# Kernel optimization log

Hardware: AMD Instinct MI355X
Metric: run time of the kernel (lower is better)

The kernel has to match this reference:

```python
import jax, jax.numpy as jnp
import numpy as np

N = 50000      # num_nodes
E = 800000     # num_edges (avg degree 16)
D = 128        # input_dim = hidden_dim = output_dim
L = 3          # num_layers
EPS = 1e-5     # BatchNorm eps


def setup_inputs() -> dict:
    key = jax.random.key(0)
    k_x, k_e, k_w, k_b = jax.random.split(key, 4)
    x = jax.random.normal(k_x, (N, D), dtype=jnp.float32)
    edge_index = jax.random.randint(k_e, (2, E), 0, N, dtype=jnp.int32)
    # Stacked per-layer params: GCN weight/bias + BatchNorm gamma/beta
    Ws = jax.random.normal(k_w, (L, D, D), dtype=jnp.float32) * (1.0 / np.sqrt(D))
    bs = jax.random.normal(k_b, (L, D), dtype=jnp.float32) * 0.01
    gammas = jnp.ones((L, D), dtype=jnp.float32)
    betas = jnp.zeros((L, D), dtype=jnp.float32)
    return {"x": x, "edge_index": edge_index, "Ws": Ws, "bs": bs,
            "gammas": gammas, "betas": betas}


def reference(x, edge_index, Ws, bs, gammas, betas):
    """CausalGNN forward: L x (GCNConv -> BN(train stats) -> ReLU[not last]) with residuals.
    Dropout p=0 (deterministic). GCNConv is PyG-style: add self-loops, symmetric
    D^{-1/2} (A+I) D^{-1/2} normalization, linear transform + bias."""
    src, dst = edge_index[0], edge_index[1]
    # degree including self-loop (+1), computed at aggregation index
    deg = jax.ops.segment_sum(jnp.ones((E,), jnp.float32), dst, num_segments=N) + 1.0
    dis = jax.lax.rsqrt(deg)                       # deg >= 1, safe
    norm = dis[src] * dis[dst]                      # [E] edge norm
    self_norm = dis * dis                           # [N] self-loop norm = 1/deg

    for i in range(L):
        h = x @ Ws[i]                               # [N, D]
        # scatter-add aggregation of normalized neighbor messages
        agg = jax.ops.segment_sum(h[src] * norm[:, None], dst, num_segments=N)
        agg = agg + self_norm[:, None] * h + bs[i]
        # BatchNorm1d (training mode: biased batch statistics over nodes)
        mean = jnp.mean(agg, axis=0)
        var = jnp.mean(jnp.square(agg - mean), axis=0)
        y = gammas[i] * (agg - mean) * jax.lax.rsqrt(var + EPS) + betas[i]
        if i < L - 1:
            y = jax.nn.relu(y)
        x = x + y if i > 0 else y                   # residual (dims match)
    return x
```

## Files before the change

### kernel.cpp

```cpp
#include <hip/hip_runtime.h>
#include <hip/hip_bf16.h>
#include <hip/hip_fp16.h>

#define N_ 50000
#define E_ 800000
#define D_ 128
#define L_ 3

#define GG 782
#define CB 3125

typedef _Float16 half8 __attribute__((ext_vector_type(8)));
typedef float f32x4 __attribute__((ext_vector_type(4)));


__device__ inline float4 hcvt(uint2 u) {
    __half2 h0 = *(__half2*)&u.x;
    __half2 h1 = *(__half2*)&u.y;
    float2 f0 = __half22float2(h0);
    float2 f1 = __half22float2(h1);
    return make_float4(f0.x, f0.y, f1.x, f1.y);
}

__device__ inline unsigned pkh(float a, float b) {
    __half2 h = __floats2half2_rn(a, b);
    return *(unsigned*)&h;
}

__device__ inline unsigned short pkh1(float a) {
    _Float16 h = (_Float16)a;
    return *(unsigned short*)&h;
}


__global__ void k_countw(const int* __restrict__ dst, int* __restrict__ deg,
                         int* __restrict__ offbuf,
                         const float* __restrict__ Ws, unsigned short* __restrict__ Wb) {
    int b = blockIdx.x;
    if (b < CB) {
        int e = b * 256 + threadIdx.x;
        offbuf[e] = atomicAdd(&deg[dst[e]], 1);
    } else {
        int l = b - CB;
        const float* Wl = Ws + l * 16384;
        unsigned short* Wo = Wb + l * 16384;
        for (int i = threadIdx.x; i < 16384; i += 256) {
            int n = i >> 7, k = i & 127;
            Wo[n * 128 + k] = pkh1(Wl[k * 128 + n]);
        }
    }
}


__global__ __launch_bounds__(1024) void k_scan1(const int* __restrict__ deg,
                                                int* __restrict__ linc,
                                                int* __restrict__ bsum,
                                                float* __restrict__ dis) {
    __shared__ int wsum[16];
    int t    = threadIdx.x;
    int lane = t & 63;
    int wid  = t >> 6;
    int i    = blockIdx.x * 1024 + t;
    int d    = (i < N_) ? deg[i] : 0;
    if (i < N_) dis[i] = rsqrtf((float)d + 1.0f);
    int v = d;
#pragma unroll
    for (int off = 1; off < 64; off <<= 1) {
        int u = __shfl_up(v, off);
        if (lane >= off) v += u;
    }
    if (lane == 63) wsum[wid] = v;
    __syncthreads();
    if (wid == 0) {
        int w = (lane < 16) ? wsum[lane] : 0;
#pragma unroll
        for (int off = 1; off < 16; off <<= 1) {
            int u = __shfl_up(w, off);
            if (lane >= off) w += u;
        }
        if (lane < 16) wsum[lane] = w;
    }
    __syncthreads();
    int woff = (wid > 0) ? wsum[wid - 1] : 0;
    v += woff;
    if (i < N_) linc[i] = v;
    if (t == 1023) bsum[blockIdx.x] = v;
}

__global__ __launch_bounds__(1024) void k_scan3(const int* __restrict__ linc,
                                                const int* __restrict__ bsum,
                                                int* __restrict__ row_ptr) {
    __shared__ int sboff;
    int t = threadIdx.x;
    if (t < 64) {
        int v = (t < 49) ? bsum[t] : 0;
#pragma unroll
        for (int off = 1; off < 64; off <<= 1) {
            int u = __shfl_up(v, off);
            if (t >= off) v += u;
        }
        int ex = (blockIdx.x == 0) ? 0 : __shfl(v, (int)blockIdx.x - 1, 64);
        if (t == 0) sboff = ex;
    }
    __syncthreads();
    int i = blockIdx.x * 1024 + t;
    if (i < N_) row_ptr[i + 1] = linc[i] + sboff;
    if (i == 0) row_ptr[0] = 0;
}


__device__ __forceinline__ void gemm_body(const float* __restrict__ Xin,
                                          const unsigned short* __restrict__ Wb,
                                          const float* __restrict__ dis,
                                          uint4* __restrict__ Hb,
                                          const float* __restrict__ st,
                                          const float* __restrict__ gamma,
                                          const float* __restrict__ beta,
                                          const unsigned short* __restrict__ resH,
                                          unsigned short* __restrict__ xoutH,
                                          int blk) {
    __shared__ unsigned short wt[128 * 136];
    __shared__ unsigned short xb[64 * 136];
    __shared__ float sab[256];
    int t  = threadIdx.x;
    int r0 = blk * 64;

    if (st) {
        if (t < 128) {
            float s = 0.f, s2 = 0.f;
#pragma unroll
            for (int k = 0; k < 8; ++k) {
                s  += st[k * 256 + t];
                s2 += st[k * 256 + 128 + t];
            }
            float mean = s * (1.0f / N_);
            float var  = s2 * (1.0f / N_) - mean * mean;
            float a = gamma[t] * rsqrtf(var + 1e-5f);
            sab[t]       = a;
            sab[128 + t] = beta[t] - mean * a;
        }
        __syncthreads();
    }

#pragma unroll
    for (int j = 0; j < 8; ++j) {
        int i = t + 256 * j;
        int row = i >> 4, c16 = i & 15;
        *(uint4*)&wt[row * 136 + c16 * 8] = ((const uint4*)Wb)[i];
    }
#pragma unroll
    for (int j = 0; j < 8; ++j) {
        int g   = t + 256 * j;
        int row = g >> 5;
        int c4  = (g & 31) * 4;
        int gr  = r0 + row;
        float4 v = make_float4(0.f, 0.f, 0.f, 0.f);
        if (gr < N_) {
            v = *(const float4*)(Xin + gr * 128 + c4);
            if (st) {
                v.x = fmaxf(sab[c4] * v.x + sab[128 + c4], 0.f);
                v.y = fmaxf(sab[c4 + 1] * v.y + sab[128 + c4 + 1], 0.f);
                v.z = fmaxf(sab[c4 + 2] * v.z + sab[128 + c4 + 2], 0.f);
                v.w = fmaxf(sab[c4 + 3] * v.w + sab[128 + c4 + 3], 0.f);
                if (resH) {
                    float4 rr = hcvt(*(const uint2*)(resH + gr * 128 + c4));
                    v.x += rr.x; v.y += rr.y; v.z += rr.z; v.w += rr.w;
                }
            }
        }
        uint2 p;
        p.x = pkh(v.x, v.y);
        p.y = pkh(v.z, v.w);
        if (st && gr < N_) *(uint2*)(xoutH + gr * 128 + c4) = p;
        *(uint2*)&xb[row * 136 + c4] = p;
    }
    __syncthreads();

    int wv   = t >> 6;
    int lane = t & 63;
    int ln   = lane & 15;
    int quad = lane >> 4;

    const unsigned short* arow = &xb[(wv * 16 + ln) * 136 + quad * 8];
    half8 af[4];
#pragma unroll
    for (int ks = 0; ks < 4; ++ks) af[ks] = *(const half8*)(arow + ks * 32);

    f32x4 acc[8];
#pragma unroll
    for (int ct = 0; ct < 8; ++ct) acc[ct] = (f32x4){0.f, 0.f, 0.f, 0.f};

#pragma unroll
    for (int ct = 0; ct < 8; ++ct) {
        const unsigned short* wp = &wt[(ct * 16 + ln) * 136 + quad * 8];
#pragma unroll
        for (int ks = 0; ks < 4; ++ks) {
            half8 bf = *(const half8*)(wp + ks * 32);
            acc[ct] = __builtin_amdgcn_mfma_f32_16x16x32_f16(af[ks], bf, acc[ct], 0, 0, 0);
        }
    }

    float dr[4];
#pragma unroll
    for (int reg = 0; reg < 4; ++reg) {
        int r = r0 + wv * 16 + quad * 4 + reg;
        dr[reg] = dis[r < N_ ? r : (N_ - 1)];
    }
    __syncthreads();
#pragma unroll
    for (int ct = 0; ct < 8; ++ct) {
#pragma unroll
        for (int reg = 0; reg < 4; ++reg) {
            int lrow = wv * 16 + quad * 4 + reg;
            xb[lrow * 136 + ct * 16 + ln] = pkh1(acc[ct][reg] * dr[reg]);
        }
    }
    __syncthreads();
#pragma unroll
    for (int j = 0; j < 4; ++j) {
        int i = t + 256 * j;
        int row = i >> 4, c16 = i & 15;
        int gr = r0 + row;
        if (gr < N_) Hb[gr * 16 + c16] = *(uint4*)&xb[row * 136 + c16 * 8];
    }
}


__global__ __launch_bounds__(256) void k_fillg(const int* __restrict__ src,
                                               const int* __restrict__ dst,
                                               const int* __restrict__ row_ptr,
                                               const int* __restrict__ offbuf,
                                               int* __restrict__ csr_src,
                                               const float* __restrict__ x,
                                               const unsigned short* __restrict__ Wb,
                                               const float* __restrict__ dis,
                                               uint4* __restrict__ Hb) {
    int b = blockIdx.x;
    if (b < GG) {
        gemm_body(x, Wb, dis, Hb, nullptr, nullptr, nullptr, nullptr, nullptr, b);
    } else {
        int e = (b - GG) * 256 + threadIdx.x;
        int d = dst[e];
        csr_src[row_ptr[d] + offbuf[e]] = src[e];
    }
}


__global__ __launch_bounds__(256) void k_gemm(const float* __restrict__ Xin,
                                              const unsigned short* __restrict__ Wb,
                                              const float* __restrict__ dis,
                                              uint4* __restrict__ Hb,
                                              const float* __restrict__ st,
                                              const float* __restrict__ gamma,
                                              const float* __restrict__ beta,
                                              const unsigned short* __restrict__ resH,
                                              unsigned short* __restrict__ xoutH) {
    gemm_body(Xin, Wb, dis, Hb, st, gamma, beta, resH, xoutH, blockIdx.x);
}


__global__ __launch_bounds__(256) void k_agg(const uint4* __restrict__ Hb,
                                             const int* __restrict__ row_ptr,
                                             const int* __restrict__ csr_src,
                                             const float* __restrict__ dis,
                                             const float* __restrict__ bias,
                                             float4* __restrict__ AGG,
                                             float* __restrict__ stats2) {
    int tid  = threadIdx.x;
    int sub  = tid >> 4;
    int lane = tid & 15;
    int node = blockIdx.x * 16 + sub;

    int beg = row_ptr[node], end = row_ptr[node + 1];
    uint4 su = Hb[node * 16 + lane];
    float4 acc0 = hcvt(make_uint2(su.x, su.y));
    float4 acc1 = hcvt(make_uint2(su.z, su.w));

    for (int c = beg; c < end; c += 16) {
        int m = end - c; if (m > 16) m = 16;
        int idx = (lane < m) ? csr_src[c + lane] : 0;
        int j = 0;
        for (; j + 4 <= m; j += 4) {
            int s0 = __shfl(idx, j, 16);
            int s1 = __shfl(idx, j + 1, 16);
            int s2 = __shfl(idx, j + 2, 16);
            int s3 = __shfl(idx, j + 3, 16);
            uint4 a0 = Hb[s0 * 16 + lane];
            uint4 a1 = Hb[s1 * 16 + lane];
            uint4 a2 = Hb[s2 * 16 + lane];
            uint4 a3 = Hb[s3 * 16 + lane];
            float4 f00 = hcvt(make_uint2(a0.x, a0.y)), f01 = hcvt(make_uint2(a0.z, a0.w));
            float4 f10 = hcvt(make_uint2(a1.x, a1.y)), f11 = hcvt(make_uint2(a1.z, a1.w));
            float4 f20 = hcvt(make_uint2(a2.x, a2.y)), f21 = hcvt(make_uint2(a2.z, a2.w));
            float4 f30 = hcvt(make_uint2(a3.x, a3.y)), f31 = hcvt(make_uint2(a3.z, a3.w));
            acc0.x += f00.x + f10.x + f20.x + f30.x;
            acc0.y += f00.y + f10.y + f20.y + f30.y;
            acc0.z += f00.z + f10.z + f20.z + f30.z;
            acc0.w += f00.w + f10.w + f20.w + f30.w;
            acc1.x += f01.x + f11.x + f21.x + f31.x;
            acc1.y += f01.y + f11.y + f21.y + f31.y;
            acc1.z += f01.z + f11.z + f21.z + f31.z;
            acc1.w += f01.w + f11.w + f21.w + f31.w;
        }
        for (; j < m; ++j) {
            int s0 = __shfl(idx, j, 16);
            uint4 a0 = Hb[s0 * 16 + lane];
            float4 f00 = hcvt(make_uint2(a0.x, a0.y)), f01 = hcvt(make_uint2(a0.z, a0.w));
            acc0.x += f00.x; acc0.y += f00.y; acc0.z += f00.z; acc0.w += f00.w;
            acc1.x += f01.x; acc1.y += f01.y; acc1.z += f01.z; acc1.w += f01.w;
        }
    }

    float dn = dis[node];
    float4 b0 = *(const float4*)(bias + lane * 8);
    float4 b1 = *(const float4*)(bias + lane * 8 + 4);
    float4 r0, r1;
    r0.x = dn * acc0.x + b0.x; r0.y = dn * acc0.y + b0.y;
    r0.z = dn * acc0.z + b0.z; r0.w = dn * acc0.w + b0.w;
    r1.x = dn * acc1.x + b1.x; r1.y = dn * acc1.y + b1.y;
    r1.z = dn * acc1.z + b1.z; r1.w = dn * acc1.w + b1.w;
    AGG[node * 32 + lane * 2]     = r0;
    AGG[node * 32 + lane * 2 + 1] = r1;

    __shared__ float sbuf[16][128];
    float4* sp = (float4*)&sbuf[sub][lane * 8];
    sp[0] = r0; sp[1] = r1;
    __syncthreads();
    if (tid < 128) {
        float s = 0.f, s2 = 0.f;
#pragma unroll
        for (int k = 0; k < 16; ++k) {
            float v = sbuf[k][tid];
            s += v; s2 += v * v;
        }
        float* stp = stats2 + (blockIdx.x & 7) * 256;
        atomicAdd(&stp[tid], s);
        atomicAdd(&stp[128 + tid], s2);
    }
}


__global__ __launch_bounds__(256) void k_normF(const float4* __restrict__ AGG,
                                               const unsigned short* __restrict__ resH,
                                               const float* __restrict__ st,
                                               const float* __restrict__ gamma,
                                               const float* __restrict__ beta,
                                               float4* __restrict__ OUT) {
    __shared__ float sab[256];
    int t = threadIdx.x;
    if (t < 128) {
        float s = 0.f, s2 = 0.f;
#pragma unroll
        for (int k = 0; k < 8; ++k) {
            s  += st[k * 256 + t];
            s2 += st[k * 256 + 128 + t];
        }
        float mean = s * (1.0f / N_);
        float var  = s2 * (1.0f / N_) - mean * mean;
        float a = gamma[t] * rsqrtf(var + 1e-5f);
        sab[t]       = a;
        sab[128 + t] = beta[t] - mean * a;
    }
    __syncthreads();
    for (int i = blockIdx.x * 256 + t; i < N_ * 32; i += gridDim.x * 256) {
        int f4 = (i & 31) * 4;
        float4 v = AGG[i];
        float4 rr = hcvt(((const uint2*)resH)[i]);
        v.x = sab[f4] * v.x + sab[128 + f4] + rr.x;
        v.y = sab[f4 + 1] * v.y + sab[128 + f4 + 1] + rr.y;
        v.z = sab[f4 + 2] * v.z + sab[128 + f4 + 2] + rr.z;
        v.w = sab[f4 + 3] * v.w + sab[128 + f4 + 3] + rr.w;
        OUT[i] = v;
    }
}


extern "C" void kernel_launch(void* const* d_in, const int* in_sizes, int n_in,
                              void* d_out, int out_size, void* d_ws, size_t ws_size,
                              hipStream_t stream) {
    const float* x      = (const float*)d_in[0];
    const int*   ei     = (const int*)d_in[1];
    const float* Ws     = (const float*)d_in[2];
    const float* bs     = (const float*)d_in[3];
    const float* gammas = (const float*)d_in[4];
    const float* betas  = (const float*)d_in[5];
    float* out = (float*)d_out;

    const int* src = ei;
    const int* dst = ei + E_;

    char* w = (char*)d_ws;
    int*   deg     = (int*)(w + 0);
    float* stats2  = (float*)(w + 200000);
    int*   row_ptr = (int*)(w + 224576);
    float* dis     = (float*)(w + 424592);
    int*   offbuf  = (int*)(w + 624592);
    int*   csr_src = (int*)(w + 3824592);
    uint4* Hb      = (uint4*)(w + 7024640);
    unsigned short* XBh = (unsigned short*)(w + 19824640);
    unsigned short* Wb  = (unsigned short*)(w + 32624640);
    float* AGG     = out;

    int* linc = (int*)XBh;
    int* bsum = (int*)XBh + N_;

    hipMemsetAsync(d_ws, 0, 224576, stream);

    k_countw<<<CB + 3, 256, 0, stream>>>(dst, deg, offbuf, Ws, Wb);
    k_scan1<<<49, 1024, 0, stream>>>(deg, linc, bsum, dis);
    k_scan3<<<49, 1024, 0, stream>>>(linc, bsum, row_ptr);
    k_fillg<<<GG + CB, 256, 0, stream>>>(src, dst, row_ptr, offbuf, csr_src,
                                         x, Wb, dis, Hb);

    k_agg<<<N_ / 16, 256, 0, stream>>>(Hb, row_ptr, csr_src, dis, bs,
                                       (float4*)AGG, stats2);
    k_gemm<<<GG, 256, 0, stream>>>(AGG, Wb + 16384, dis, Hb,
                                   stats2, gammas, betas, nullptr, XBh);
    k_agg<<<N_ / 16, 256, 0, stream>>>(Hb, row_ptr, csr_src, dis, bs + D_,
                                       (float4*)AGG, stats2 + 2048);
    k_gemm<<<GG, 256, 0, stream>>>(AGG, Wb + 32768, dis, Hb,
                                   stats2 + 2048, gammas + D_, betas + D_, XBh, XBh);
    k_agg<<<N_ / 16, 256, 0, stream>>>(Hb, row_ptr, csr_src, dis, bs + 2 * D_,
                                       (float4*)AGG, stats2 + 4096);
    k_normF<<<1024, 256, 0, stream>>>((const float4*)AGG, XBh,
                                      stats2 + 4096, gammas + 2 * D_, betas + 2 * D_,
                                      (float4*)out);
}
```

Baseline: 292.9 us.

## Store aggregation output in fp16 workspace and unroll neighbor gather by eight

The per-layer aggregation result is now packed to fp16 in a dedicated workspace buffer instead of being written as fp32 into the output. The following GEMM and the final normalization kernel read it as fp16, which halves that intermediate traffic. BN statistics are still computed from the fp32 values before packing. Separately, the neighbor gather loop gains an 8-wide unrolled path to keep more loads in flight. The cost is extra fp16 rounding of the pre-BatchNorm activations.

After: 295.9 us. No clear change (+1.0%).

```diff
diff --git a/kernel.cpp b/kernel.cpp
--- a/kernel.cpp
+++ b/kernel.cpp
@@ -110,6 +110,7 @@
 
 
 __device__ __forceinline__ void gemm_body(const float* __restrict__ Xin,
+                                          const unsigned short* __restrict__ XinH,
                                           const unsigned short* __restrict__ Wb,
                                           const float* __restrict__ dis,
                                           uint4* __restrict__ Hb,
@@ -156,7 +157,8 @@
         int gr  = r0 + row;
         float4 v = make_float4(0.f, 0.f, 0.f, 0.f);
         if (gr < N_) {
-            v = *(const float4*)(Xin + gr * 128 + c4);
+            if (XinH) v = hcvt(*(const uint2*)(XinH + gr * 128 + c4));
+            else      v = *(const float4*)(Xin + gr * 128 + c4);
             if (st) {
                 v.x = fmaxf(sab[c4] * v.x + sab[128 + c4], 0.f);
                 v.y = fmaxf(sab[c4 + 1] * v.y + sab[128 + c4 + 1], 0.f);
@@ -237,7 +239,7 @@
                                                uint4* __restrict__ Hb) {
     int b = blockIdx.x;
     if (b < GG) {
-        gemm_body(x, Wb, dis, Hb, nullptr, nullptr, nullptr, nullptr, nullptr, b);
+        gemm_body(x, nullptr, Wb, dis, Hb, nullptr, nullptr, nullptr, nullptr, nullptr, b);
     } else {
         int e = (b - GG) * 256 + threadIdx.x;
         int d = dst[e];
@@ -246,7 +248,7 @@
 }
 
 
-__global__ __launch_bounds__(256) void k_gemm(const float* __restrict__ Xin,
+__global__ __launch_bounds__(256) void k_gemm(const unsigned short* __restrict__ XinH,
                                               const unsigned short* __restrict__ Wb,
                                               const float* __restrict__ dis,
                                               uint4* __restrict__ Hb,
@@ -255,7 +257,7 @@
                                               const float* __restrict__ beta,
                                               const unsigned short* __restrict__ resH,
                                               unsigned short* __restrict__ xoutH) {
-    gemm_body(Xin, Wb, dis, Hb, st, gamma, beta, resH, xoutH, blockIdx.x);
+    gemm_body(nullptr, XinH, Wb, dis, Hb, st, gamma, beta, resH, xoutH, blockIdx.x);
 }
 
 
@@ -264,7 +266,7 @@
                                              const int* __restrict__ csr_src,
                                              const float* __restrict__ dis,
                                              const float* __restrict__ bias,
-                                             float4* __restrict__ AGG,
+                                             uint4* __restrict__ AGGh,
                                              float* __restrict__ stats2) {
     int tid  = threadIdx.x;
     int sub  = tid >> 4;
@@ -280,6 +282,40 @@
         int m = end - c; if (m > 16) m = 16;
         int idx = (lane < m) ? csr_src[c + lane] : 0;
         int j = 0;
+        for (; j + 8 <= m; j += 8) {
+            int s0 = __shfl(idx, j, 16);
+            int s1 = __shfl(idx, j + 1, 16);
+            int s2 = __shfl(idx, j + 2, 16);
+            int s3 = __shfl(idx, j + 3, 16);
+            int s4 = __shfl(idx, j + 4, 16);
+            int s5 = __shfl(idx, j + 5, 16);
+            int s6 = __shfl(idx, j + 6, 16);
+            int s7 = __shfl(idx, j + 7, 16);
+            uint4 a0 = Hb[s0 * 16 + lane];
+            uint4 a1 = Hb[s1 * 16 + lane];
+            uint4 a2 = Hb[s2 * 16 + lane];
+            uint4 a3 = Hb[s3 * 16 + lane];
+            uint4 a4 = Hb[s4 * 16 + lane];
+            uint4 a5 = Hb[s5 * 16 + lane];
+            uint4 a6 = Hb[s6 * 16 + lane];
+            uint4 a7 = Hb[s7 * 16 + lane];
+            float4 f00 = hcvt(make_uint2(a0.x, a0.y)), f01 = hcvt(make_uint2(a0.z, a0.w));
+            float4 f10 = hcvt(make_uint2(a1.x, a1.y)), f11 = hcvt(make_uint2(a1.z, a1.w));
+            float4 f20 = hcvt(make_uint2(a2.x, a2.y)), f21 = hcvt(make_uint2(a2.z, a2.w));
+            float4 f30 = hcvt(make_uint2(a3.x, a3.y)), f31 = hcvt(make_uint2(a3.z, a3.w));
+            float4 f40 = hcvt(make_uint2(a4.x, a4.y)), f41 = hcvt(make_uint2(a4.z, a4.w));
+            float4 f50 = hcvt(make_uint2(a5.x, a5.y)), f51 = hcvt(make_uint2(a5.z, a5.w));
+            float4 f60 = hcvt(make_uint2(a6.x, a6.y)), f61 = hcvt(make_uint2(a6.z, a6.w));
+            float4 f70 = hcvt(make_uint2(a7.x, a7.y)), f71 = hcvt(make_uint2(a7.z, a7.w));
+            acc0.x += (f00.x + f10.x) + (f20.x + f30.x) + (f40.x + f50.x) + (f60.x + f70.x);
+            acc0.y += (f00.y + f10.y) + (f20.y + f30.y) + (f40.y + f50.y) + (f60.y + f70.y);
+            acc0.z += (f00.z + f10.z) + (f20.z + f30.z) + (f40.z + f50.z) + (f60.z + f70.z);
+            acc0.w += (f00.w + f10.w) + (f20.w + f30.w) + (f40.w + f50.w) + (f60.w + f70.w);
+            acc1.x += (f01.x + f11.x) + (f21.x + f31.x) + (f41.x + f51.x) + (f61.x + f71.x);
+            acc1.y += (f01.y + f11.y) + (f21.y + f31.y) + (f41.y + f51.y) + (f61.y + f71.y);
+            acc1.z += (f01.z + f11.z) + (f21.z + f31.z) + (f41.z + f51.z) + (f61.z + f71.z);
+            acc1.w += (f01.w + f11.w) + (f21.w + f31.w) + (f41.w + f51.w) + (f61.w + f71.w);
+        }
         for (; j + 4 <= m; j += 4) {
             int s0 = __shfl(idx, j, 16);
             int s1 = __shfl(idx, j + 1, 16);
@@ -319,8 +355,10 @@
     r0.z = dn * acc0.z + b0.z; r0.w = dn * acc0.w + b0.w;
     r1.x = dn * acc1.x + b1.x; r1.y = dn * acc1.y + b1.y;
     r1.z = dn * acc1.z + b1.z; r1.w = dn * acc1.w + b1.w;
-    AGG[node * 32 + lane * 2]     = r0;
-    AGG[node * 32 + lane * 2 + 1] = r1;
+    uint4 o;
+    o.x = pkh(r0.x, r0.y); o.y = pkh(r0.z, r0.w);
+    o.z = pkh(r1.x, r1.y); o.w = pkh(r1.z, r1.w);
+    AGGh[node * 16 + lane] = o;
 
     __shared__ float sbuf[16][128];
     float4* sp = (float4*)&sbuf[sub][lane * 8];
@@ -340,8 +378,8 @@
 }
 
 
-__global__ __launch_bounds__(256) void k_normF(const float4* __restrict__ AGG,
-                                               const unsigned short* __restrict__ resH,
+__global__ __launch_bounds__(256) void k_normF(const uint4* __restrict__ AGGh,
+                                               const uint4* __restrict__ resH,
                                                const float* __restrict__ st,
                                                const float* __restrict__ gamma,
                                                const float* __restrict__ beta,
@@ -362,15 +400,23 @@
         sab[128 + t] = beta[t] - mean * a;
     }
     __syncthreads();
-    for (int i = blockIdx.x * 256 + t; i < N_ * 32; i += gridDim.x * 256) {
-        int f4 = (i & 31) * 4;
-        float4 v = AGG[i];
-        float4 rr = hcvt(((const uint2*)resH)[i]);
-        v.x = sab[f4] * v.x + sab[128 + f4] + rr.x;
-        v.y = sab[f4 + 1] * v.y + sab[128 + f4 + 1] + rr.y;
-        v.z = sab[f4 + 2] * v.z + sab[128 + f4 + 2] + rr.z;
-        v.w = sab[f4 + 3] * v.w + sab[128 + f4 + 3] + rr.w;
-        OUT[i] = v;
+    for (int i = blockIdx.x * 256 + t; i < N_ * 16; i += gridDim.x * 256) {
+        int f8 = (i & 15) * 8;
+        uint4 va = AGGh[i];
+        uint4 vr = resH[i];
+        float4 a0 = hcvt(make_uint2(va.x, va.y)), a1 = hcvt(make_uint2(va.z, va.w));
+        float4 q0 = hcvt(make_uint2(vr.x, vr.y)), q1 = hcvt(make_uint2(vr.z, vr.w));
+        float4 o0, o1;
+        o0.x = sab[f8] * a0.x + sab[128 + f8] + q0.x;
+        o0.y = sab[f8 + 1] * a0.y + sab[128 + f8 + 1] + q0.y;
+        o0.z = sab[f8 + 2] * a0.z + sab[128 + f8 + 2] + q0.z;
+        o0.w = sab[f8 + 3] * a0.w + sab[128 + f8 + 3] + q0.w;
+        o1.x = sab[f8 + 4] * a1.x + sab[128 + f8 + 4] + q1.x;
+        o1.y = sab[f8 + 5] * a1.y + sab[128 + f8 + 5] + q1.y;
+        o1.z = sab[f8 + 6] * a1.z + sab[128 + f8 + 6] + q1.z;
+        o1.w = sab[f8 + 7] * a1.w + sab[128 + f8 + 7] + q1.w;
+        OUT[i * 2]     = o0;
+        OUT[i * 2 + 1] = o1;
     }
 }
 
@@ -399,7 +445,7 @@
     uint4* Hb      = (uint4*)(w + 7024640);
     unsigned short* XBh = (unsigned short*)(w + 19824640);
     unsigned short* Wb  = (unsigned short*)(w + 32624640);
-    float* AGG     = out;
+    uint4* AGGh    = (uint4*)(w + 32723072);
 
     int* linc = (int*)XBh;
     int* bsum = (int*)XBh + N_;
@@ -413,16 +459,16 @@
                                          x, Wb, dis, Hb);
 
     k_agg<<<N_ / 16, 256, 0, stream>>>(Hb, row_ptr, csr_src, dis, bs,
-                                       (float4*)AGG, stats2);
-    k_gemm<<<GG, 256, 0, stream>>>(AGG, Wb + 16384, dis, Hb,
+                                       AGGh, stats2);
+    k_gemm<<<GG, 256, 0, stream>>>((const unsigned short*)AGGh, Wb + 16384, dis, Hb,
                                    stats2, gammas, betas, nullptr, XBh);
     k_agg<<<N_ / 16, 256, 0, stream>>>(Hb, row_ptr, csr_src, dis, bs + D_,
-                                       (float4*)AGG, stats2 + 2048);
-    k_gemm<<<GG, 256, 0, stream>>>(AGG, Wb + 32768, dis, Hb,
+                                       AGGh, stats2 + 2048);
+    k_gemm<<<GG, 256, 0, stream>>>((const unsigned short*)AGGh, Wb + 32768, dis, Hb,
                                    stats2 + 2048, gammas + D_, betas + D_, XBh, XBh);
     k_agg<<<N_ / 16, 256, 0, stream>>>(Hb, row_ptr, csr_src, dis, bs + 2 * D_,
-                                       (float4*)AGG, stats2 + 4096);
-    k_normF<<<1024, 256, 0, stream>>>((const float4*)AGG, XBh,
+                                       AGGh, stats2 + 4096);
+    k_normF<<<1024, 256, 0, stream>>>(AGGh, (const uint4*)XBh,
                                       stats2 + 4096, gammas + 2 * D_, betas + 2 * D_,
                                       (float4*)out);
 }
```
